# Kernel tuning notes

Measured on AMD Instinct MI355X. Metric: run time of the kernel, lower is better.

## Reference

```python
import jax, jax.numpy as jnp
import numpy as np

N_NODES = 50000
N_EDGES = 800000
IN_CH = 512
HIDDEN = 512


def setup_inputs() -> dict:
    key = jax.random.key(0)
    k1, k2, k3, k4 = jax.random.split(key, 4)
    x = jax.random.normal(k1, (N_NODES, IN_CH), dtype=jnp.float32)
    edge_index = jax.random.randint(k2, (2, N_EDGES), 0, N_NODES, dtype=jnp.int64)
    # Glorot-style scaling for weights
    W1 = jax.random.normal(k3, (IN_CH, HIDDEN), dtype=jnp.float32) / np.sqrt(IN_CH)
    b1 = jnp.zeros((HIDDEN,), dtype=jnp.float32)
    W2 = jax.random.normal(k4, (HIDDEN, 1), dtype=jnp.float32) / np.sqrt(HIDDEN)
    b2 = jnp.zeros((1,), dtype=jnp.float32)
    return {"x": x, "edge_index": edge_index, "W1": W1, "b1": b1, "W2": W2, "b2": b2}


def _gcn_conv(x, edge_index, W, b):
    """PyG GCNConv: add self-loops, symmetric D^{-1/2}(A+I)D^{-1/2} normalization."""
    N = x.shape[0]
    xw = x @ W                                   # [N, out]
    row, col = edge_index[0], edge_index[1]      # source -> target
    # degree on target nodes, +1 for the self-loop
    deg = jax.ops.segment_sum(jnp.ones_like(col, dtype=xw.dtype), col, num_segments=N) + 1.0
    dis = jax.lax.rsqrt(deg)                     # deg^{-1/2}, [N]
    norm = dis[row] * dis[col]                   # [E]
    agg = jax.ops.segment_sum(norm[:, None] * xw[row], col, num_segments=N)
    agg = agg + (dis * dis)[:, None] * xw        # self-loop contribution
    return agg + b


def reference(x, edge_index, W1, b1, W2, b2):
    h = jax.nn.relu(_gcn_conv(x, edge_index, W1, b1))
    # dropout in eval mode (training=False) -> identity
    out = _gcn_conv(h, edge_index, W2, b2)
    return out.squeeze(-1)                       # [N]
```

## Files before the change

kernel.cpp:

```cpp
#include <hip/hip_runtime.h>

#define IN_CH 512
#define SCAN_BLK 1024

typedef _Float16 f16x8 __attribute__((ext_vector_type(8)));
typedef float f32x4 __attribute__((ext_vector_type(4)));

__device__ __forceinline__ void gload_lds16(const void* g, void* l) {
    __builtin_amdgcn_global_load_lds(
        (const __attribute__((address_space(1))) unsigned int*)g,
        (__attribute__((address_space(3))) unsigned int*)l, 16, 0, 0);
}

__global__ __launch_bounds__(256) void k_merged1(const float* __restrict__ W1,
                                                 _Float16* __restrict__ W1t,
                                                 const int* __restrict__ col,
                                                 int* __restrict__ deg, int E, int N) {
    __shared__ float tile[32][33];
    if ((int)blockIdx.x >= 256) {
        int e = ((int)blockIdx.x - 256) * 256 + threadIdx.x;
        if (e < E) {
            int d = col[e];
            if ((unsigned)d < (unsigned)N) atomicAdd(&deg[d], 1);
        }
        return;
    }
    const int bk = (blockIdx.x & 15) * 32, bn = (blockIdx.x >> 4) * 32;
    const int tx = threadIdx.x & 31, ty = threadIdx.x >> 5;
#pragma unroll
    for (int p = 0; p < 4; ++p)
        tile[ty + p * 8][tx] = W1[(size_t)(bk + ty + p * 8) * 512 + bn + tx];
    __syncthreads();
#pragma unroll
    for (int p = 0; p < 4; ++p)
        W1t[(size_t)(bn + ty + p * 8) * 512 + bk + tx] = (_Float16)tile[tx][ty + p * 8];
}

__global__ __launch_bounds__(SCAN_BLK) void k_psum(const int* __restrict__ deg,
                                                   int* __restrict__ bsum, int N) {
    __shared__ int red[SCAN_BLK / 64];
    int i = blockIdx.x * SCAN_BLK + threadIdx.x;
    int v = (i < N) ? deg[i] : 0;
#pragma unroll
    for (int off = 32; off > 0; off >>= 1) v += __shfl_down(v, off);
    if ((threadIdx.x & 63) == 0) red[threadIdx.x >> 6] = v;
    __syncthreads();
    if (threadIdx.x == 0) {
        int s = 0;
#pragma unroll
        for (int u = 0; u < SCAN_BLK / 64; ++u) s += red[u];
        bsum[blockIdx.x] = s;
    }
}

__global__ __launch_bounds__(SCAN_BLK) void k_write(const int* __restrict__ deg,
                                                    const int* __restrict__ bsum,
                                                    int* __restrict__ rp,
                                                    float* __restrict__ dis,
                                                    int* __restrict__ cursor, int N) {
    __shared__ int sums[SCAN_BLK];
    __shared__ int boff_s, tot_s;
    int t = threadIdx.x;
    if (t < 64) {
        int v = (t < (int)gridDim.x) ? bsum[t] : 0;
        int pre = (t < (int)blockIdx.x) ? v : 0;
        int a = pre, b = v;
#pragma unroll
        for (int off = 32; off > 0; off >>= 1) {
            a += __shfl_down(a, off);
            b += __shfl_down(b, off);
        }
        if (t == 0) { boff_s = a; tot_s = b; }
    }
    int i = blockIdx.x * SCAN_BLK + t;
    int d = (i < N) ? deg[i] : 0;
    sums[t] = d;
    __syncthreads();
    for (int off = 1; off < SCAN_BLK; off <<= 1) {
        int u = (t >= off) ? sums[t - off] : 0;
        __syncthreads();
        sums[t] += u;
        __syncthreads();
    }
    if (i < N) {
        rp[i] = boff_s + sums[t] - d;
        dis[i] = rsqrtf((float)d + 1.0f);
        cursor[i] = 0;
    }
    if (blockIdx.x == gridDim.x - 1 && t == 0) rp[N] = tot_s;
}

__global__ __launch_bounds__(512, 4) void k_merged2(const float* __restrict__ A,
                                                    const _Float16* __restrict__ Bt,
                                                    const float* __restrict__ dis,
                                                    _Float16* __restrict__ C,
                                                    int Nrows, int nbm, int nwg,
                                                    const int* __restrict__ ei,
                                                    const int* __restrict__ rp,
                                                    int* __restrict__ cursor,
                                                    int* __restrict__ csrc,
                                                    int E, int N) {
    __shared__ __align__(16) _Float16 As[128 * 64];
    __shared__ __align__(16) _Float16 Bs[256 * 64];

    if ((int)blockIdx.x >= nwg) {
        int e = ((int)blockIdx.x - nwg) * 512 + threadIdx.x;
        if (e < E) {
            int s = ei[e];
            int d = ei[E + e];
            if ((unsigned)s < (unsigned)N && (unsigned)d < (unsigned)N) {
                int pos = atomicAdd(&cursor[d], 1);
                csrc[rp[d] + pos] = s;
            }
        }
        return;
    }

    const int g = (int)blockIdx.x;
    const int t = threadIdx.x;
    const int lane = t & 63, w = t >> 6;
    const int wm = w >> 2, wn = w & 3;

    const int q = nwg >> 3, r = nwg & 7;
    const int xcd = g & 7, within = g >> 3;
    const int wg = (xcd < r ? xcd * (q + 1) : r * (q + 1) + (xcd - r) * q) + within;
    const int bm = (wg >> 1) * 128, bn = (wg & 1) * 256;

    const int rr = lane & 15, kg = lane >> 4;
    const int lrow = lane >> 3;
    const int scol = ((lane & 7) ^ lrow) * 8;
    const int rsw = rr & 7;
    const int arow = t >> 3;
    const int achk = t & 7;
    const int agcol = (achk ^ (arow & 7)) * 8;

    const float* Abase[2];
#pragma unroll
    for (int p = 0; p < 2; ++p) {
        int grow = bm + p * 64 + arow;
        if (grow >= Nrows) grow = Nrows - 1;
        Abase[p] = A + (size_t)grow * 512 + agcol;
    }

    f32x4 acc[4][4];
#pragma unroll
    for (int i = 0; i < 4; ++i)
#pragma unroll
        for (int j = 0; j < 4; ++j) acc[i][j] = (f32x4)0.0f;

    for (int k0 = 0; k0 < 512; k0 += 64) {
#pragma unroll
        for (int p = 0; p < 4; ++p) {
            const int row = p * 64 + w * 8 + lrow;
            gload_lds16(Bt + (size_t)(bn + row) * 512 + k0 + scol,
                        Bs + (p * 64 + w * 8) * 64);
        }
#pragma unroll
        for (int p = 0; p < 2; ++p) {
            const float* gp = Abase[p] + k0;
            float4 u0 = *(const float4*)gp;
            float4 u1 = *(const float4*)(gp + 4);
            f16x8 o;
            o[0] = (_Float16)u0.x; o[1] = (_Float16)u0.y;
            o[2] = (_Float16)u0.z; o[3] = (_Float16)u0.w;
            o[4] = (_Float16)u1.x; o[5] = (_Float16)u1.y;
            o[6] = (_Float16)u1.z; o[7] = (_Float16)u1.w;
            *(f16x8*)(As + (p * 64 + arow) * 64 + achk * 8) = o;
        }
        __syncthreads();
#pragma unroll
        for (int kk = 0; kk < 2; ++kk) {
            f16x8 a[4], b[4];
#pragma unroll
            for (int i = 0; i < 4; ++i)
                a[i] = *(const f16x8*)(As + (wm * 64 + i * 16 + rr) * 64 +
                                       (((kk << 2) + kg) ^ rsw) * 8);
#pragma unroll
            for (int j = 0; j < 4; ++j)
                b[j] = *(const f16x8*)(Bs + (wn * 64 + j * 16 + rr) * 64 +
                                       (((kk << 2) + kg) ^ rsw) * 8);
#pragma unroll
            for (int i = 0; i < 4; ++i)
#pragma unroll
                for (int j = 0; j < 4; ++j)
                    acc[i][j] = __builtin_amdgcn_mfma_f32_16x16x32_f16(a[i], b[j], acc[i][j], 0, 0, 0);
        }
        __syncthreads();
    }

#pragma unroll
    for (int i = 0; i < 4; ++i)
#pragma unroll
        for (int reg = 0; reg < 4; ++reg) {
            int m = bm + wm * 64 + i * 16 + kg * 4 + reg;
            int mc = (m < Nrows) ? m : Nrows - 1;
            float dm = dis[mc];
#pragma unroll
            for (int j = 0; j < 4; ++j) {
                int n = bn + wn * 64 + j * 16 + rr;
                C[(size_t)m * 512 + n] = (_Float16)(acc[i][j][reg] * dm);
            }
        }
}

__global__ __launch_bounds__(256) void k_agg(const _Float16* __restrict__ y,
                                             const float* __restrict__ dis,
                                             const int* __restrict__ rp,
                                             const int* __restrict__ csrc,
                                             const float* __restrict__ b1,
                                             const float* __restrict__ W2,
                                             float* __restrict__ z, int N) {
    const int n = blockIdx.x * 4 + (threadIdx.x >> 6);
    if (n >= N) return;
    const int l = threadIdx.x & 63;

    const float d1 = dis[n];
    f16x8 self = *(const f16x8*)(y + (size_t)n * 512 + l * 8);
    float acc[8];
#pragma unroll
    for (int c = 0; c < 8; ++c) acc[c] = (float)self[c];

    int j = rp[n], jend = rp[n + 1];
    for (; j + 8 <= jend; j += 8) {
        int s[8]; f16x8 v[8];
#pragma unroll
        for (int u = 0; u < 8; ++u) s[u] = csrc[j + u];
#pragma unroll
        for (int u = 0; u < 8; ++u)
            v[u] = *(const f16x8*)(y + (size_t)s[u] * 512 + l * 8);
#pragma unroll
        for (int u = 0; u < 8; ++u)
#pragma unroll
            for (int c = 0; c < 8; ++c) acc[c] += (float)v[u][c];
    }
    for (; j + 2 <= jend; j += 2) {
        int s0 = csrc[j], s1 = csrc[j + 1];
        f16x8 v0 = *(const f16x8*)(y + (size_t)s0 * 512 + l * 8);
        f16x8 v1 = *(const f16x8*)(y + (size_t)s1 * 512 + l * 8);
#pragma unroll
        for (int c = 0; c < 8; ++c) acc[c] += (float)v0[c] + (float)v1[c];
    }
    if (j < jend) {
        f16x8 v0 = *(const f16x8*)(y + (size_t)csrc[j] * 512 + l * 8);
#pragma unroll
        for (int c = 0; c < 8; ++c) acc[c] += (float)v0[c];
    }

    float4 bb0 = *(const float4*)(b1 + l * 8);
    float4 bb1 = *(const float4*)(b1 + l * 8 + 4);
    float4 w20 = *(const float4*)(W2 + l * 8);
    float4 w21 = *(const float4*)(W2 + l * 8 + 4);
    float bbv[8] = {bb0.x, bb0.y, bb0.z, bb0.w, bb1.x, bb1.y, bb1.z, bb1.w};
    float w2v[8] = {w20.x, w20.y, w20.z, w20.w, w21.x, w21.y, w21.z, w21.w};
    float p = 0.0f;
#pragma unroll
    for (int c = 0; c < 8; ++c) {
        float h = fmaxf(acc[c] * d1 + bbv[c], 0.0f);
        p += h * w2v[c];
    }
#pragma unroll
    for (int off = 32; off > 0; off >>= 1) p += __shfl_down(p, off);
    if (l == 0) z[n] = d1 * p;
}

__global__ void k_out(const float* __restrict__ z, const float* __restrict__ dis,
                      const int* __restrict__ rp, const int* __restrict__ csrc,
                      const float* __restrict__ b2, float* __restrict__ out, int N) {
    int n = blockIdx.x * blockDim.x + threadIdx.x;
    if (n >= N) return;
    float acc = z[n];
    int j = rp[n], jend = rp[n + 1];
    for (; j + 4 <= jend; j += 4) {
        float a0 = z[csrc[j]];
        float a1 = z[csrc[j + 1]];
        float a2 = z[csrc[j + 2]];
        float a3 = z[csrc[j + 3]];
        acc += (a0 + a1) + (a2 + a3);
    }
    for (; j < jend; ++j) acc += z[csrc[j]];
    out[n] = dis[n] * acc + b2[0];
}

extern "C" void kernel_launch(void* const* d_in, const int* in_sizes, int n_in,
                              void* d_out, int out_size, void* d_ws, size_t ws_size,
                              hipStream_t stream) {
    const float* x  = (const float*)d_in[0];
    const int*   ei = (const int*)d_in[1];
    const float* W1 = (const float*)d_in[2];
    const float* b1 = (const float*)d_in[3];
    const float* W2 = (const float*)d_in[4];
    const float* b2 = (const float*)d_in[5];
    float* out = (float*)d_out;

    const int N = in_sizes[0] / IN_CH;
    const int E = in_sizes[1] / 2;
    const int nbm = (N + 127) / 128;
    const int M2 = nbm * 128;
    const int NB = (N + SCAN_BLK - 1) / SCAN_BLK;
    const int DEGB  = (E + 255) / 256;
    const int FILLB = (E + 511) / 512;
    const int nwg   = nbm * 2;

    char* ws = (char*)d_ws;
    size_t off = 0;
    auto alloc = [&](size_t bytes) {
        char* p = ws + off;
        off += (bytes + 255) & ~(size_t)255;
        return p;
    };
    _Float16* y   = (_Float16*)alloc((size_t)M2 * 512 * sizeof(_Float16));
    _Float16* W1t = (_Float16*)alloc((size_t)512 * 512 * sizeof(_Float16));
    int*   deg    = (int*)alloc((size_t)N * sizeof(int));
    float* dis    = (float*)alloc((size_t)N * sizeof(float));
    int*   rp     = (int*)alloc((size_t)(N + 1) * sizeof(int));
    int*   cursor = (int*)alloc((size_t)N * sizeof(int));
    int*   csrc   = (int*)alloc((size_t)E * sizeof(int));
    float* z      = (float*)alloc((size_t)N * sizeof(float));
    int*   bsum   = (int*)alloc((size_t)64 * sizeof(int));

    hipMemsetAsync(deg, 0, (size_t)N * sizeof(int), stream);

    k_merged1<<<256 + DEGB, 256, 0, stream>>>(W1, W1t, ei + E, deg, E, N);
    k_psum<<<NB, SCAN_BLK, 0, stream>>>(deg, bsum, N);
    k_write<<<NB, SCAN_BLK, 0, stream>>>(deg, bsum, rp, dis, cursor, N);
    k_merged2<<<nwg + FILLB, 512, 0, stream>>>(x, W1t, dis, y, N, nbm, nwg,
                                               ei, rp, cursor, csrc, E, N);
    k_agg<<<(N + 3) / 4, 256, 0, stream>>>(y, dis, rp, csrc, b1, W2, z, N);
    k_out<<<(N + 255) / 256, 256, 0, stream>>>(z, dis, rp, csrc, b2, out, N);
}
```

Baseline: 238.0 us.

## Fuse scan kernels, vectorize degree counting, prefetch GEMM A tiles into registers

Degree counting now reads the target indices as int4, issuing four atomics per thread, which cuts the block count and the number of load instructions. The separate block-sum kernel is merged into the scan kernel: each block recomputes all block totals redundantly, which removes one launch and its global round trip. The GEMM main loop loads the next k-slice of A from global memory into registers before the current slice's MFMAs run, so the load latency overlaps with compute at the cost of extra registers. The int4 path assumes E is divisible by 4 and that col is 16-byte aligned; any tail edges would be dropped.

```diff
diff --git a/kernel.cpp b/kernel.cpp
--- a/kernel.cpp
+++ b/kernel.cpp
@@ -15,13 +15,16 @@
 __global__ __launch_bounds__(256) void k_merged1(const float* __restrict__ W1,
                                                  _Float16* __restrict__ W1t,
                                                  const int* __restrict__ col,
-                                                 int* __restrict__ deg, int E, int N) {
+                                                 int* __restrict__ deg, int E4, int N) {
     __shared__ float tile[32][33];
     if ((int)blockIdx.x >= 256) {
-        int e = ((int)blockIdx.x - 256) * 256 + threadIdx.x;
-        if (e < E) {
-            int d = col[e];
-            if ((unsigned)d < (unsigned)N) atomicAdd(&deg[d], 1);
+        int e4 = ((int)blockIdx.x - 256) * 256 + threadIdx.x;
+        if (e4 < E4) {
+            int4 d4 = ((const int4*)col)[e4];
+            if ((unsigned)d4.x < (unsigned)N) atomicAdd(&deg[d4.x], 1);
+            if ((unsigned)d4.y < (unsigned)N) atomicAdd(&deg[d4.y], 1);
+            if ((unsigned)d4.z < (unsigned)N) atomicAdd(&deg[d4.z], 1);
+            if ((unsigned)d4.w < (unsigned)N) atomicAdd(&deg[d4.w], 1);
         }
         return;
     }
@@ -36,33 +39,32 @@
         W1t[(size_t)(bn + ty + p * 8) * 512 + bk + tx] = (_Float16)tile[tx][ty + p * 8];
 }
 
-__global__ __launch_bounds__(SCAN_BLK) void k_psum(const int* __restrict__ deg,
-                                                   int* __restrict__ bsum, int N) {
-    __shared__ int red[SCAN_BLK / 64];
-    int i = blockIdx.x * SCAN_BLK + threadIdx.x;
-    int v = (i < N) ? deg[i] : 0;
-#pragma unroll
-    for (int off = 32; off > 0; off >>= 1) v += __shfl_down(v, off);
-    if ((threadIdx.x & 63) == 0) red[threadIdx.x >> 6] = v;
-    __syncthreads();
-    if (threadIdx.x == 0) {
-        int s = 0;
-#pragma unroll
-        for (int u = 0; u < SCAN_BLK / 64; ++u) s += red[u];
-        bsum[blockIdx.x] = s;
-    }
-}
-
-__global__ __launch_bounds__(SCAN_BLK) void k_write(const int* __restrict__ deg,
-                                                    const int* __restrict__ bsum,
-                                                    int* __restrict__ rp,
-                                                    float* __restrict__ dis,
-                                                    int* __restrict__ cursor, int N) {
+__global__ __launch_bounds__(SCAN_BLK) void k_scan(const int* __restrict__ deg,
+                                                   int* __restrict__ rp,
+                                                   float* __restrict__ dis,
+                                                   int* __restrict__ cursor, int N) {
+    __shared__ int tsum[64];
     __shared__ int sums[SCAN_BLK];
     __shared__ int boff_s, tot_s;
-    int t = threadIdx.x;
+    const int t = threadIdx.x;
+    const int nb = gridDim.x;
+    const int wv = t >> 6, ln = t & 63;
+
+    for (int j = wv; j < nb; j += 16) {
+        int base = j * SCAN_BLK;
+        int s = 0;
+#pragma unroll
+        for (int qq = 0; qq < SCAN_BLK / 64; ++qq) {
+            int idx = base + qq * 64 + ln;
+            s += (idx < N) ? deg[idx] : 0;
+        }
+#pragma unroll
+        for (int off = 32; off > 0; off >>= 1) s += __shfl_down(s, off);
+        if (ln == 0) tsum[j] = s;
+    }
+    __syncthreads();
     if (t < 64) {
-        int v = (t < (int)gridDim.x) ? bsum[t] : 0;
+        int v = (t < nb) ? tsum[t] : 0;
         int pre = (t < (int)blockIdx.x) ? v : 0;
         int a = pre, b = v;
 #pragma unroll
@@ -141,6 +143,12 @@
         if (grow >= Nrows) grow = Nrows - 1;
         Abase[p] = A + (size_t)grow * 512 + agcol;
     }
+    float4 pa[2], pb[2];
+#pragma unroll
+    for (int p = 0; p < 2; ++p) {
+        pa[p] = *(const float4*)(Abase[p]);
+        pb[p] = *(const float4*)(Abase[p] + 4);
+    }
 
     f32x4 acc[4][4];
 #pragma unroll
@@ -157,17 +165,21 @@
         }
 #pragma unroll
         for (int p = 0; p < 2; ++p) {
-            const float* gp = Abase[p] + k0;
-            float4 u0 = *(const float4*)gp;
-            float4 u1 = *(const float4*)(gp + 4);
             f16x8 o;
-            o[0] = (_Float16)u0.x; o[1] = (_Float16)u0.y;
-            o[2] = (_Float16)u0.z; o[3] = (_Float16)u0.w;
-            o[4] = (_Float16)u1.x; o[5] = (_Float16)u1.y;
-            o[6] = (_Float16)u1.z; o[7] = (_Float16)u1.w;
+            o[0] = (_Float16)pa[p].x; o[1] = (_Float16)pa[p].y;
+            o[2] = (_Float16)pa[p].z; o[3] = (_Float16)pa[p].w;
+            o[4] = (_Float16)pb[p].x; o[5] = (_Float16)pb[p].y;
+            o[6] = (_Float16)pb[p].z; o[7] = (_Float16)pb[p].w;
             *(f16x8*)(As + (p * 64 + arow) * 64 + achk * 8) = o;
         }
         __syncthreads();
+        if (k0 + 64 < 512) {
+#pragma unroll
+            for (int p = 0; p < 2; ++p) {
+                pa[p] = *(const float4*)(Abase[p] + k0 + 64);
+                pb[p] = *(const float4*)(Abase[p] + k0 + 68);
+            }
+        }
 #pragma unroll
         for (int kk = 0; kk < 2; ++kk) {
             f16x8 a[4], b[4];
@@ -297,7 +309,8 @@
     const int nbm = (N + 127) / 128;
     const int M2 = nbm * 128;
     const int NB = (N + SCAN_BLK - 1) / SCAN_BLK;
-    const int DEGB  = (E + 255) / 256;
+    const int E4 = E / 4;
+    const int DEGB4 = (E4 + 255) / 256;
     const int FILLB = (E + 511) / 512;
     const int nwg   = nbm * 2;
 
@@ -316,13 +329,11 @@
     int*   cursor = (int*)alloc((size_t)N * sizeof(int));
     int*   csrc   = (int*)alloc((size_t)E * sizeof(int));
     float* z      = (float*)alloc((size_t)N * sizeof(float));
-    int*   bsum   = (int*)alloc((size_t)64 * sizeof(int));
 
     hipMemsetAsync(deg, 0, (size_t)N * sizeof(int), stream);
 
-    k_merged1<<<256 + DEGB, 256, 0, stream>>>(W1, W1t, ei + E, deg, E, N);
-    k_psum<<<NB, SCAN_BLK, 0, stream>>>(deg, bsum, N);
-    k_write<<<NB, SCAN_BLK, 0, stream>>>(deg, bsum, rp, dis, cursor, N);
+    k_merged1<<<256 + DEGB4, 256, 0, stream>>>(W1, W1t, ei + E, deg, E4, N);
+    k_scan<<<NB, SCAN_BLK, 0, stream>>>(deg, rp, dis, cursor, N);
     k_merged2<<<nwg + FILLB, 512, 0, stream>>>(x, W1t, dis, y, N, nbm, nwg,
                                                ei, rp, cursor, csrc, E, N);
     k_agg<<<(N + 3) / 4, 256, 0, stream>>>(y, dis, rp, csrc, b1, W2, z, N);
```

Result: no change. 239.7 us (+0.7%).
